# Kernel optimization log

Measured on AMD Instinct MI355X. Metric: run time of the kernel, lower is better.

Reference implementation:

```python
import jax, jax.numpy as jnp
import numpy as np

B, S, HQ, HKV, DH = 1, 2048, 32, 8, 128
DE = HQ * DH  # DEmbed = 4096
G = HQ // HKV  # GQA group size = 4


def apply_rope(x, cs):
    # x: [B, S, H, DH]; cs: [2, S, 1, DH//2] (broadcast over B via leading dims)
    d = x.shape[-1] // 2
    x1, x2 = x[..., :d], x[..., d:]
    y1 = x1 * cs[0] + x2 * cs[1]
    y2 = -x1 * cs[1] + x2 * cs[0]
    return jnp.concatenate([y1, y2], axis=-1)


def setup_inputs() -> dict:
    key = jax.random.key(0)
    ks = jax.random.split(key, 5)
    x = jax.random.normal(ks[0], (B, S, DE), dtype=jnp.float32)
    # Precomputed rotary tables, shaped [2, S, 1, DH//2] so they broadcast over [B,S,H,DH//2]
    half = DH // 2
    inv_freq = 1.0 / (10000.0 ** (np.arange(half, dtype=np.float64) / half))
    ang = np.arange(S, dtype=np.float64)[:, None] * inv_freq[None, :]
    cos_sin_RoPE = jnp.asarray(
        np.stack([np.cos(ang), np.sin(ang)])[:, :, None, :], dtype=jnp.float32
    )
    sc = DE ** -0.5
    wq = jax.random.normal(ks[1], (DE, HQ * DH), dtype=jnp.float32) * sc
    wk = jax.random.normal(ks[2], (DE, HKV * DH), dtype=jnp.float32) * sc
    wv = jax.random.normal(ks[3], (DE, HKV * DH), dtype=jnp.float32) * sc
    wo = jax.random.normal(ks[4], (DE, DE), dtype=jnp.float32) * sc
    return {"x": x, "cos_sin_RoPE": cos_sin_RoPE, "wq": wq, "wk": wk, "wv": wv, "wo": wo}


def reference(x, cos_sin_RoPE, wq, wk, wv, wo):
    b, s, _ = x.shape
    q = (x @ wq).reshape(b, s, HQ, DH)
    k = (x @ wk).reshape(b, s, HKV, DH)
    v = (x @ wv).reshape(b, s, HKV, DH)
    q = apply_rope(q, cos_sin_RoPE)
    k = apply_rope(k, cos_sin_RoPE)
    # GQA causal SDPA: group query heads per kv head
    q = q.transpose(0, 2, 1, 3).reshape(b, HKV, G, s, DH)  # [b,kv,g,s,d]
    k = k.transpose(0, 2, 1, 3)  # [b,kv,s,d]
    v = v.transpose(0, 2, 1, 3)  # [b,kv,s,d]
    scale = DH ** -0.5
    scores = jnp.einsum('bkgsd,bktd->bkgst', q, k) * scale  # [b,kv,g,s,s]
    mask = jnp.tril(jnp.ones((s, s), dtype=bool))
    scores = jnp.where(mask, scores, jnp.finfo(scores.dtype).min)
    p = jax.nn.softmax(scores, axis=-1)
    o = jnp.einsum('bkgst,bktd->bkgsd', p, v)  # [b,kv,g,s,d]
    o = o.transpose(0, 3, 1, 2, 4).reshape(b, s, HQ * DH)
    return o @ wo
```

## Files before the change

### kernel.cpp

```cpp
#include <hip/hip_runtime.h>
#include <hip/hip_bf16.h>
#include <cstdint>
#include <cstddef>

typedef __bf16 bf16x8 __attribute__((ext_vector_type(8)));
typedef float floatx4 __attribute__((ext_vector_type(4)));

#define MFMA(a, b, c) __builtin_amdgcn_mfma_f32_16x16x32_bf16((a), (b), (c), 0, 0, 0)
#define WAITVM(N) asm volatile("s_waitcnt vmcnt(" #N ")" ::: "memory")
#define WAITLGKM0() asm volatile("s_waitcnt lgkmcnt(0)" ::: "memory")
#define BARRIER() do { asm volatile("" ::: "memory"); __builtin_amdgcn_s_barrier(); asm volatile("" ::: "memory"); } while (0)
#define SCHEDBAR() __builtin_amdgcn_sched_barrier(0)

__device__ __forceinline__ unsigned short f2bf(float f) {
  unsigned u = __builtin_bit_cast(unsigned, f);
  u += 0x7fffu + ((u >> 16) & 1u);
  return (unsigned short)(u >> 16);
}
__device__ __forceinline__ float bf2f(unsigned short h) {
  unsigned u = ((unsigned)h) << 16;
  return __builtin_bit_cast(float, u);
}
__device__ __forceinline__ float fast_exp2(float x) {
#if __has_builtin(__builtin_amdgcn_exp2f)
  return __builtin_amdgcn_exp2f(x);
#else
  return exp2f(x);
#endif
}

__device__ __forceinline__ void gl2lds16(const unsigned short* g, unsigned short* l) {
  __builtin_amdgcn_global_load_lds(
      (const __attribute__((address_space(1))) unsigned int*)g,
      (__attribute__((address_space(3))) unsigned int*)l, 16, 0, 0);
}

__global__ void convert_f32_bf16(const float* __restrict__ src,
                                 unsigned short* __restrict__ dst, int n4) {
  int i = blockIdx.x * 256 + threadIdx.x;
  if (i >= n4) return;
  float4 f = ((const float4*)src)[i];
  ushort4 o;
  o.x = f2bf(f.x); o.y = f2bf(f.y); o.z = f2bf(f.z); o.w = f2bf(f.w);
  ((ushort4*)dst)[i] = o;
}

__global__ void transpose_f32_bf16(const float* __restrict__ src,
                                   unsigned short* __restrict__ dst, int K, int N) {
  __shared__ float tile[64 * 65];
  int tn = blockIdx.x * 64, tk = blockIdx.y * 64;
  int r = threadIdx.x >> 4;
  int c4 = (threadIdx.x & 15) * 4;
#pragma unroll
  for (int i = 0; i < 4; i++) {
    float4 f = *(const float4*)&src[(size_t)(tk + r + 16 * i) * N + tn + c4];
    float* tr = &tile[(r + 16 * i) * 65 + c4];
    tr[0] = f.x; tr[1] = f.y; tr[2] = f.z; tr[3] = f.w;
  }
  __syncthreads();
#pragma unroll
  for (int i = 0; i < 4; i++) {
    ushort4 o;
    o.x = f2bf(tile[(c4 + 0) * 65 + r + 16 * i]);
    o.y = f2bf(tile[(c4 + 1) * 65 + r + 16 * i]);
    o.z = f2bf(tile[(c4 + 2) * 65 + r + 16 * i]);
    o.w = f2bf(tile[(c4 + 3) * 65 + r + 16 * i]);
    *(ushort4*)&dst[(size_t)(tn + r + 16 * i) * K + tk + c4] = o;
  }
}

template <int MI, int NI, bool F32OUT>
__global__ __launch_bounds__(512, 2) void gemm_pipe(
    const unsigned short* __restrict__ A,
    const unsigned short* __restrict__ Bt,
    void* __restrict__ C, int M, int N, int K) {
  constexpr int BM = MI * 32;
  constexpr int BN = NI * 64;
  constexpr int NCA = BM / 64;
  __shared__ alignas(16) unsigned short Al[2][BM * 64];
  __shared__ alignas(16) unsigned short Bl[2][BN * 64];
  const int tid = threadIdx.x;
  const int w = tid >> 6, L = tid & 63;
  const int lr = L & 15, lg = L >> 4, lr7 = lr & 7;
  const int bm = blockIdx.y * BM, bn = blockIdx.x * BN;
  const int wm = (w >> 2) * (MI * 16);
  const int wn = (w & 3) * (NI * 16);
  const int NT = K >> 6;

  const int srow = tid >> 3, scg = tid & 7;
  const unsigned short* Ag = &A[(size_t)(bm + srow) * K + ((scg ^ (srow & 7)) * 8)];
  const unsigned short* Bg = &Bt[(size_t)(bn + srow) * K + ((scg ^ (srow & 7)) * 8)];
  unsigned short* AlT = &Al[0][0] + tid * 8;
  unsigned short* BlT = &Bl[0][0] + tid * 8;

#pragma unroll
  for (int t = 0; t < 2; ++t) {
#pragma unroll
    for (int c = 0; c < NCA; ++c)
      gl2lds16(Ag + (size_t)(c * 64) * K + t * 64, AlT + t * (BM * 64) + c * 4096);
#pragma unroll
    for (int c = 0; c < NI; ++c)
      gl2lds16(Bg + (size_t)(c * 64) * K + t * 64, BlT + t * (BN * 64) + c * 4096);
  }

  floatx4 acc[MI][NI] = {};

#define CLUSTER(MLO, KK)                                                    \
  do {                                                                      \
    __builtin_amdgcn_s_setprio(1);                                          \
    _Pragma("unroll") for (int mi = 0; mi < 4; ++mi)                        \
        _Pragma("unroll") for (int ni = 0; ni < NI; ++ni)                   \
            acc[(MLO) + mi][ni] =                                           \
        MFMA(af[(MLO) + mi][KK], bq[ni][KK], acc[(MLO) + mi][ni]);          \
    __builtin_amdgcn_s_setprio(0);                                          \
  } while (0)

  if constexpr (NCA + NI == 7) WAITVM(7); else WAITVM(6);
  BARRIER();

  for (int T = 0; T < NT; ++T) {
    const int buf = T & 1;
    const unsigned short* Ab = &Al[buf][0];
    const unsigned short* Bb = &Bl[buf][0];
    const bool st = (T + 2) < NT;
    const size_t kofs = (size_t)(T + 2) * 64;
    unsigned short* Ad = AlT + buf * (BM * 64);
    unsigned short* Bd = BlT + buf * (BN * 64);

    bf16x8 af[MI][2], bq[NI][2];
#pragma unroll
    for (int mi = 0; mi < MI; ++mi) {
      af[mi][0] = *(const bf16x8*)&Ab[(wm + mi * 16 + lr) * 64 + ((lg ^ lr7) * 8)];
      af[mi][1] = *(const bf16x8*)&Ab[(wm + mi * 16 + lr) * 64 + (((4 + lg) ^ lr7) * 8)];
    }
#pragma unroll
    for (int ni = 0; ni < NI; ++ni) {
      bq[ni][0] = *(const bf16x8*)&Bb[(wn + ni * 16 + lr) * 64 + ((lg ^ lr7) * 8)];
      bq[ni][1] = *(const bf16x8*)&Bb[(wn + ni * 16 + lr) * 64 + (((4 + lg) ^ lr7) * 8)];
    }

    if constexpr (MI == 8) {
      CLUSTER(0, 0);
      WAITLGKM0();
      BARRIER(); SCHEDBAR();
      if (st) {
        gl2lds16(Ag + kofs, Ad);
        gl2lds16(Ag + (size_t)64 * K + kofs, Ad + 4096);
        gl2lds16(Ag + (size_t)128 * K + kofs, Ad + 2 * 4096);
      }
      CLUSTER(4, 0);
      BARRIER(); SCHEDBAR();
      if (st) {
        gl2lds16(Ag + (size_t)192 * K + kofs, Ad + 3 * 4096);
        gl2lds16(Bg + kofs, Bd);
        if constexpr (NI >= 2) gl2lds16(Bg + (size_t)64 * K + kofs, Bd + 4096);
      }
      CLUSTER(0, 1);
      BARRIER(); SCHEDBAR();
      if (st) {
#pragma unroll
        for (int c = 2; c < NI; ++c)
          gl2lds16(Bg + (size_t)(c * 64) * K + kofs, Bd + c * 4096);
      }
      CLUSTER(4, 1);
      if constexpr (NCA + NI == 7) { if (st) { WAITVM(7); } else if (T + 1 < NT) { WAITVM(0); } }
      else                         { if (st) { WAITVM(6); } else if (T + 1 < NT) { WAITVM(0); } }
      BARRIER(); SCHEDBAR();
    } else {
      CLUSTER(0, 0);
      WAITLGKM0();
      BARRIER(); SCHEDBAR();
      if (st) {
#pragma unroll
        for (int c = 0; c < NCA; ++c)
          gl2lds16(Ag + (size_t)(c * 64) * K + kofs, Ad + c * 4096);
#pragma unroll
        for (int c = 0; c < NI; ++c)
          gl2lds16(Bg + (size_t)(c * 64) * K + kofs, Bd + c * 4096);
      }
      CLUSTER(0, 1);
      if constexpr (NCA + NI == 7) { if (st) { WAITVM(7); } else if (T + 1 < NT) { WAITVM(0); } }
      else                         { if (st) { WAITVM(6); } else if (T + 1 < NT) { WAITVM(0); } }
      BARRIER(); SCHEDBAR();
    }
  }
#undef CLUSTER

#pragma unroll
  for (int mi = 0; mi < MI; ++mi) {
#pragma unroll
    for (int ni = 0; ni < NI; ++ni) {
#pragma unroll
      for (int r = 0; r < 4; ++r) {
        size_t row = bm + wm + mi * 16 + lg * 4 + r;
        size_t col = bn + wn + ni * 16 + lr;
        float v = acc[mi][ni][r];
        if constexpr (F32OUT) ((float*)C)[row * N + col] = v;
        else ((unsigned short*)C)[row * N + col] = f2bf(v);
      }
    }
  }
}

__global__ void rope_kernel(unsigned short* __restrict__ X, const float* __restrict__ cs,
                            int H, int rowStride, int colOff, float scale) {
  int idx = blockIdx.x * 256 + threadIdx.x;
  int dg = idx & 15;
  int h = (idx >> 4) % H;
  int s = idx / (16 * H);
  size_t base = (size_t)s * rowStride + colOff + (size_t)h * 128 + dg * 4;
  ushort4 xa = *(const ushort4*)&X[base];
  ushort4 xb = *(const ushort4*)&X[base + 64];
  float4 c = *(const float4*)&cs[s * 64 + dg * 4];
  float4 sn = *(const float4*)&cs[2048 * 64 + s * 64 + dg * 4];
  ushort4 oa, ob;
  {
    float x1 = bf2f(xa.x), x2 = bf2f(xb.x);
    oa.x = f2bf((x1 * c.x + x2 * sn.x) * scale);
    ob.x = f2bf((x2 * c.x - x1 * sn.x) * scale);
  }
  {
    float x1 = bf2f(xa.y), x2 = bf2f(xb.y);
    oa.y = f2bf((x1 * c.y + x2 * sn.y) * scale);
    ob.y = f2bf((x2 * c.y - x1 * sn.y) * scale);
  }
  {
    float x1 = bf2f(xa.z), x2 = bf2f(xb.z);
    oa.z = f2bf((x1 * c.z + x2 * sn.z) * scale);
    ob.z = f2bf((x2 * c.z - x1 * sn.z) * scale);
  }
  {
    float x1 = bf2f(xa.w), x2 = bf2f(xb.w);
    oa.w = f2bf((x1 * c.w + x2 * sn.w) * scale);
    ob.w = f2bf((x2 * c.w - x1 * sn.w) * scale);
  }
  *(ushort4*)&X[base] = oa;
  *(ushort4*)&X[base + 64] = ob;
}

__global__ void v_transpose(const unsigned short* __restrict__ QKV,
                            unsigned short* __restrict__ Vt) {
  __shared__ unsigned short tile[32][33];
  int h = blockIdx.z;
  int s0 = blockIdx.x * 32, d0 = blockIdx.y * 32;
  int c = threadIdx.x & 31, r0 = threadIdx.x >> 5;
#pragma unroll
  for (int i = 0; i < 32; i += 8)
    tile[r0 + i][c] = QKV[(size_t)(s0 + r0 + i) * 6144 + 5120 + h * 128 + d0 + c];
  __syncthreads();
#pragma unroll
  for (int i = 0; i < 32; i += 8)
    Vt[(size_t)(h * 128 + d0 + r0 + i) * 2048 + s0 + c] = tile[c][r0 + i];
}

__global__ __launch_bounds__(256) void flash_kernel(
    const unsigned short* __restrict__ QKV,
    const unsigned short* __restrict__ Vt,
    unsigned short* __restrict__ O) {
  constexpr int PSTR = 72;
  __shared__ alignas(16) unsigned short Klds[64 * 128];
  __shared__ alignas(16) unsigned short Vlds[128 * 64];
  __shared__ alignas(16) unsigned short Plds[4 * 32 * PSTR];
  const int tid = threadIdx.x, w = tid >> 6, L = tid & 63;
  const int lr = L & 15, lg = L >> 4;
  const int bid = blockIdx.x;
  const int hk = bid & 7;
  const int hp = (bid >> 3) & 1;
  const int qb = 31 - (bid >> 4);
  const int hq = hk * 4 + hp * 2 + (w & 1);
  const int qr0 = qb * 64 + (w >> 1) * 32;
  const unsigned short* Kg = QKV + 4096;

  const int k_row = tid >> 4, k_lcg = tid & 15;
  const unsigned short* KgT = &Kg[(size_t)k_row * 6144 + hk * 128 + ((k_lcg ^ (k_row & 15)) * 8)];
  unsigned short* KlT = &Klds[k_row * 128 + k_lcg * 8];
  const int v_row = tid >> 3, v_lcg = tid & 7;
  const unsigned short* VgT = &Vt[(size_t)(hk * 128 + v_row) * 2048 + ((v_lcg ^ (v_row & 7)) * 8)];
  unsigned short* VlT = &Vlds[v_row * 64 + v_lcg * 8];

  bf16x8 qf[2][4];
#pragma unroll
  for (int mi = 0; mi < 2; mi++)
#pragma unroll
    for (int c = 0; c < 4; c++)
      qf[mi][c] = *(const bf16x8*)&QKV[(size_t)(qr0 + mi * 16 + lr) * 6144 + hq * 128 + c * 32 + lg * 8];

  floatx4 oacc[2][8] = {};
  float l_lane[2][4] = {};
  unsigned short* pw = &Plds[w * 32 * PSTR];

  for (int t = 0; t <= qb; t++) {
    const int kv0 = t * 64;
    __syncthreads();
#pragma unroll
    for (int i = 0; i < 4; i++) {
      gl2lds16(KgT + (size_t)(kv0 + i * 16) * 6144, KlT + i * 16 * 128);
      gl2lds16(VgT + kv0 + (size_t)(i * 32) * 2048, VlT + i * 32 * 64);
    }
    __syncthreads();

#pragma unroll
    for (int nt = 0; nt < 4; nt++) {
      bf16x8 kf[4];
#pragma unroll
      for (int c = 0; c < 4; c++)
        kf[c] = *(const bf16x8*)&Klds[(nt * 16 + lr) * 128 + (((c * 4 + lg) ^ lr) * 8)];
      floatx4 sc[2];
#pragma unroll
      for (int mi = 0; mi < 2; mi++) {
        floatx4 a = {};
#pragma unroll
        for (int c = 0; c < 4; c++) a = MFMA(qf[mi][c], kf[c], a);
        sc[mi] = a;
      }
      if (t == qb) {
#pragma unroll
        for (int mi = 0; mi < 2; mi++)
#pragma unroll
          for (int r = 0; r < 4; r++)
            if (kv0 + nt * 16 + lr > qr0 + mi * 16 + lg * 4 + r) sc[mi][r] = -3e38f;
      }
#pragma unroll
      for (int mi = 0; mi < 2; mi++)
#pragma unroll
        for (int r = 0; r < 4; r++) {
          float p = fast_exp2(sc[mi][r]);
          l_lane[mi][r] += p;
          pw[(mi * 16 + lg * 4 + r) * PSTR + nt * 16 + lr] = f2bf(p);
        }
    }

    bf16x8 pf[2][2];
#pragma unroll
    for (int mi = 0; mi < 2; mi++)
#pragma unroll
      for (int c = 0; c < 2; c++)
        pf[mi][c] = *(const bf16x8*)&pw[(mi * 16 + lr) * PSTR + c * 32 + lg * 8];

#pragma unroll
    for (int n = 0; n < 8; n++) {
#pragma unroll
      for (int c = 0; c < 2; c++) {
        bf16x8 vf = *(const bf16x8*)&Vlds[(n * 16 + lr) * 64 + (((c * 4 + lg) ^ (lr & 7)) * 8)];
#pragma unroll
        for (int mi = 0; mi < 2; mi++) oacc[mi][n] = MFMA(pf[mi][c], vf, oacc[mi][n]);
      }
    }
  }

  float linv[2][4];
#pragma unroll
  for (int mi = 0; mi < 2; mi++)
#pragma unroll
    for (int r = 0; r < 4; r++) {
      float l = l_lane[mi][r];
      l += __shfl_xor(l, 1);
      l += __shfl_xor(l, 2);
      l += __shfl_xor(l, 4);
      l += __shfl_xor(l, 8);
      linv[mi][r] = 1.0f / l;
    }

#pragma unroll
  for (int mi = 0; mi < 2; mi++)
#pragma unroll
    for (int n = 0; n < 8; n++)
#pragma unroll
      for (int r = 0; r < 4; r++) {
        size_t row = qr0 + mi * 16 + lg * 4 + r;
        size_t col = (size_t)hq * 128 + n * 16 + lr;
        O[row * 4096 + col] = f2bf(oacc[mi][n][r] * linv[mi][r]);
      }
}

extern "C" void kernel_launch(void* const* d_in, const int* in_sizes, int n_in,
                              void* d_out, int out_size, void* d_ws, size_t ws_size,
                              hipStream_t stream) {
  const float* x  = (const float*)d_in[0];
  const float* cs = (const float*)d_in[1];
  const float* wq = (const float*)d_in[2];
  const float* wk = (const float*)d_in[3];
  const float* wv = (const float*)d_in[4];
  const float* wo = (const float*)d_in[5];
  float* out = (float*)d_out;

  char* ws = (char*)d_ws;
  unsigned short* xb   = (unsigned short*)(ws);
  unsigned short* wqt  = (unsigned short*)(ws + 16777216);
  unsigned short* wkt  = (unsigned short*)(ws + 50331648);
  unsigned short* wvt  = (unsigned short*)(ws + 58720256);
  unsigned short* wot  = (unsigned short*)(ws + 67108864);
  unsigned short* QKVb = (unsigned short*)(ws + 100663296);
  unsigned short* Vtb  = (unsigned short*)(ws + 125829120);
  unsigned short* Ob   = xb;

  convert_f32_bf16<<<8192, 256, 0, stream>>>(x, xb, 2097152);
  transpose_f32_bf16<<<dim3(64, 64), 256, 0, stream>>>(wq, wqt, 4096, 4096);
  transpose_f32_bf16<<<dim3(16, 64), 256, 0, stream>>>(wk, wkt, 4096, 1024);
  transpose_f32_bf16<<<dim3(16, 64), 256, 0, stream>>>(wv, wvt, 4096, 1024);
  transpose_f32_bf16<<<dim3(64, 64), 256, 0, stream>>>(wo, wot, 4096, 4096);

  gemm_pipe<8, 3, false><<<dim3(32, 8), 512, 0, stream>>>(xb, wqt, QKVb, 2048, 6144, 4096);

  rope_kernel<<<4096, 256, 0, stream>>>(QKVb, cs, 32, 6144, 0, 0.12751743f);
  rope_kernel<<<1024, 256, 0, stream>>>(QKVb, cs, 8, 6144, 4096, 1.0f);

  v_transpose<<<dim3(64, 4, 8), 256, 0, stream>>>(QKVb, Vtb);

  flash_kernel<<<512, 256, 0, stream>>>(QKVb, Vtb, Ob);

  gemm_pipe<4, 4, true><<<dim3(16, 16), 512, 0, stream>>>(Ob, wot, out, 2048, 4096, 4096);
}
```

Before: 488.5 us.

## Interleave LDS fragment loads with MFMA clusters and reassign warp column mapping

Restructures the GEMM main loop so LDS fragment reads are issued in stages between MFMA clusters instead of all up front. Each stage is followed by a wait and barrier, and global-to-LDS prefetches are redistributed across the stages. In the non-MI8 variant, each warp now owns strided columns (stride 64) instead of a contiguous block, and it loads B fragments one column at a time. The aim is to cut register pressure and hide LDS latency behind MFMA work, at the cost of more barriers per iteration and removed sched_barriers.

```diff
diff --git a/kernel.cpp b/kernel.cpp
--- a/kernel.cpp
+++ b/kernel.cpp
@@ -10,7 +10,6 @@
 #define WAITVM(N) asm volatile("s_waitcnt vmcnt(" #N ")" ::: "memory")
 #define WAITLGKM0() asm volatile("s_waitcnt lgkmcnt(0)" ::: "memory")
 #define BARRIER() do { asm volatile("" ::: "memory"); __builtin_amdgcn_s_barrier(); asm volatile("" ::: "memory"); } while (0)
-#define SCHEDBAR() __builtin_amdgcn_sched_barrier(0)
 
 __device__ __forceinline__ unsigned short f2bf(float f) {
   unsigned u = __builtin_bit_cast(unsigned, f);
@@ -77,6 +76,7 @@
   constexpr int BM = MI * 32;
   constexpr int BN = NI * 64;
   constexpr int NCA = BM / 64;
+  constexpr int CSTEP = (MI == 8) ? 16 : 64;
   __shared__ alignas(16) unsigned short Al[2][BM * 64];
   __shared__ alignas(16) unsigned short Bl[2][BN * 64];
   const int tid = threadIdx.x;
@@ -84,7 +84,7 @@
   const int lr = L & 15, lg = L >> 4, lr7 = lr & 7;
   const int bm = blockIdx.y * BM, bn = blockIdx.x * BN;
   const int wm = (w >> 2) * (MI * 16);
-  const int wn = (w & 3) * (NI * 16);
+  const int wn = (w & 3) * ((MI == 8) ? (NI * 16) : 16);
   const int NT = K >> 6;
 
   const int srow = tid >> 3, scg = tid & 7;
@@ -105,15 +105,8 @@
 
   floatx4 acc[MI][NI] = {};
 
-#define CLUSTER(MLO, KK)                                                    \
-  do {                                                                      \
-    __builtin_amdgcn_s_setprio(1);                                          \
-    _Pragma("unroll") for (int mi = 0; mi < 4; ++mi)                        \
-        _Pragma("unroll") for (int ni = 0; ni < NI; ++ni)                   \
-            acc[(MLO) + mi][ni] =                                           \
-        MFMA(af[(MLO) + mi][KK], bq[ni][KK], acc[(MLO) + mi][ni]);          \
-    __builtin_amdgcn_s_setprio(0);                                          \
-  } while (0)
+#define LD_A(mi, kk) (*(const bf16x8*)&Ab[(wm + (mi) * 16 + lr) * 64 + ((((kk) * 4 + lg) ^ lr7) * 8)])
+#define LD_B(ni, kk) (*(const bf16x8*)&Bb[(wn + (ni) * CSTEP + lr) * 64 + ((((kk) * 4 + lg) ^ lr7) * 8)])
 
   if constexpr (NCA + NI == 7) WAITVM(7); else WAITVM(6);
   BARRIER();
@@ -126,65 +119,121 @@
     const size_t kofs = (size_t)(T + 2) * 64;
     unsigned short* Ad = AlT + buf * (BM * 64);
     unsigned short* Bd = BlT + buf * (BN * 64);
-
     bf16x8 af[MI][2], bq[NI][2];
-#pragma unroll
-    for (int mi = 0; mi < MI; ++mi) {
-      af[mi][0] = *(const bf16x8*)&Ab[(wm + mi * 16 + lr) * 64 + ((lg ^ lr7) * 8)];
-      af[mi][1] = *(const bf16x8*)&Ab[(wm + mi * 16 + lr) * 64 + (((4 + lg) ^ lr7) * 8)];
-    }
-#pragma unroll
-    for (int ni = 0; ni < NI; ++ni) {
-      bq[ni][0] = *(const bf16x8*)&Bb[(wn + ni * 16 + lr) * 64 + ((lg ^ lr7) * 8)];
-      bq[ni][1] = *(const bf16x8*)&Bb[(wn + ni * 16 + lr) * 64 + (((4 + lg) ^ lr7) * 8)];
-    }
 
     if constexpr (MI == 8) {
-      CLUSTER(0, 0);
-      WAITLGKM0();
-      BARRIER(); SCHEDBAR();
+#pragma unroll
+      for (int mi = 0; mi < 4; ++mi) af[mi][0] = LD_A(mi, 0);
+#pragma unroll
+      for (int ni = 0; ni < NI; ++ni) bq[ni][0] = LD_B(ni, 0);
+      WAITLGKM0(); BARRIER();
+      __builtin_amdgcn_s_setprio(1);
+#pragma unroll
+      for (int mi = 0; mi < 4; ++mi)
+#pragma unroll
+        for (int ni = 0; ni < NI; ++ni)
+          acc[mi][ni] = MFMA(af[mi][0], bq[ni][0], acc[mi][ni]);
+      __builtin_amdgcn_s_setprio(0);
+#pragma unroll
+      for (int mi = 4; mi < 8; ++mi) af[mi][0] = LD_A(mi, 0);
+#pragma unroll
+      for (int ni = 0; ni < NI; ++ni) bq[ni][1] = LD_B(ni, 1);
+      WAITLGKM0(); BARRIER();
+      __builtin_amdgcn_s_setprio(1);
+#pragma unroll
+      for (int mi = 4; mi < 8; ++mi)
+#pragma unroll
+        for (int ni = 0; ni < NI; ++ni)
+          acc[mi][ni] = MFMA(af[mi][0], bq[ni][0], acc[mi][ni]);
+      __builtin_amdgcn_s_setprio(0);
+#pragma unroll
+      for (int mi = 0; mi < 8; ++mi) af[mi][1] = LD_A(mi, 1);
+      if (st) {
+#pragma unroll
+        for (int c = 0; c < NI; ++c)
+          gl2lds16(Bg + (size_t)(c * 64) * K + kofs, Bd + c * 4096);
+      }
+      WAITLGKM0(); BARRIER();
+      __builtin_amdgcn_s_setprio(1);
+#pragma unroll
+      for (int mi = 0; mi < 4; ++mi)
+#pragma unroll
+        for (int ni = 0; ni < NI; ++ni)
+          acc[mi][ni] = MFMA(af[mi][1], bq[ni][1], acc[mi][ni]);
+      __builtin_amdgcn_s_setprio(0);
+      if (st) {
+#pragma unroll
+        for (int c = 0; c < NCA; ++c)
+          gl2lds16(Ag + (size_t)(c * 64) * K + kofs, Ad + c * 4096);
+      }
+      BARRIER();
+      __builtin_amdgcn_s_setprio(1);
+#pragma unroll
+      for (int mi = 4; mi < 8; ++mi)
+#pragma unroll
+        for (int ni = 0; ni < NI; ++ni)
+          acc[mi][ni] = MFMA(af[mi][1], bq[ni][1], acc[mi][ni]);
+      __builtin_amdgcn_s_setprio(0);
+    } else {
+#pragma unroll
+      for (int mi = 0; mi < 4; ++mi) {
+        af[mi][0] = LD_A(mi, 0);
+        af[mi][1] = LD_A(mi, 1);
+      }
+      bq[0][0] = LD_B(0, 0); bq[0][1] = LD_B(0, 1);
+      WAITLGKM0(); BARRIER();
+      __builtin_amdgcn_s_setprio(1);
+#pragma unroll
+      for (int kk = 0; kk < 2; ++kk)
+#pragma unroll
+        for (int mi = 0; mi < 4; ++mi)
+          acc[mi][0] = MFMA(af[mi][kk], bq[0][kk], acc[mi][0]);
+      __builtin_amdgcn_s_setprio(0);
+      bq[1][0] = LD_B(1, 0); bq[1][1] = LD_B(1, 1);
       if (st) {
         gl2lds16(Ag + kofs, Ad);
         gl2lds16(Ag + (size_t)64 * K + kofs, Ad + 4096);
-        gl2lds16(Ag + (size_t)128 * K + kofs, Ad + 2 * 4096);
-      }
-      CLUSTER(4, 0);
-      BARRIER(); SCHEDBAR();
+        gl2lds16(Bg + kofs, Bd);
+      }
+      WAITLGKM0(); BARRIER();
+      __builtin_amdgcn_s_setprio(1);
+#pragma unroll
+      for (int kk = 0; kk < 2; ++kk)
+#pragma unroll
+        for (int mi = 0; mi < 4; ++mi)
+          acc[mi][1] = MFMA(af[mi][kk], bq[1][kk], acc[mi][1]);
+      __builtin_amdgcn_s_setprio(0);
+      bq[2][0] = LD_B(2, 0); bq[2][1] = LD_B(2, 1);
+      bq[3][0] = LD_B(3, 0); bq[3][1] = LD_B(3, 1);
+      if (st) gl2lds16(Bg + (size_t)64 * K + kofs, Bd + 4096);
+      WAITLGKM0(); BARRIER();
+      __builtin_amdgcn_s_setprio(1);
+#pragma unroll
+      for (int kk = 0; kk < 2; ++kk)
+#pragma unroll
+        for (int mi = 0; mi < 4; ++mi)
+          acc[mi][2] = MFMA(af[mi][kk], bq[2][kk], acc[mi][2]);
+      __builtin_amdgcn_s_setprio(0);
       if (st) {
-        gl2lds16(Ag + (size_t)192 * K + kofs, Ad + 3 * 4096);
-        gl2lds16(Bg + kofs, Bd);
-        if constexpr (NI >= 2) gl2lds16(Bg + (size_t)64 * K + kofs, Bd + 4096);
-      }
-      CLUSTER(0, 1);
-      BARRIER(); SCHEDBAR();
-      if (st) {
-#pragma unroll
-        for (int c = 2; c < NI; ++c)
-          gl2lds16(Bg + (size_t)(c * 64) * K + kofs, Bd + c * 4096);
-      }
-      CLUSTER(4, 1);
-      if constexpr (NCA + NI == 7) { if (st) { WAITVM(7); } else if (T + 1 < NT) { WAITVM(0); } }
-      else                         { if (st) { WAITVM(6); } else if (T + 1 < NT) { WAITVM(0); } }
-      BARRIER(); SCHEDBAR();
-    } else {
-      CLUSTER(0, 0);
-      WAITLGKM0();
-      BARRIER(); SCHEDBAR();
-      if (st) {
-#pragma unroll
-        for (int c = 0; c < NCA; ++c)
-          gl2lds16(Ag + (size_t)(c * 64) * K + kofs, Ad + c * 4096);
-#pragma unroll
-        for (int c = 0; c < NI; ++c)
-          gl2lds16(Bg + (size_t)(c * 64) * K + kofs, Bd + c * 4096);
-      }
-      CLUSTER(0, 1);
-      if constexpr (NCA + NI == 7) { if (st) { WAITVM(7); } else if (T + 1 < NT) { WAITVM(0); } }
-      else                         { if (st) { WAITVM(6); } else if (T + 1 < NT) { WAITVM(0); } }
-      BARRIER(); SCHEDBAR();
-    }
-  }
-#undef CLUSTER
+        gl2lds16(Bg + (size_t)128 * K + kofs, Bd + 2 * 4096);
+        gl2lds16(Bg + (size_t)192 * K + kofs, Bd + 3 * 4096);
+      }
+      BARRIER();
+      __builtin_amdgcn_s_setprio(1);
+#pragma unroll
+      for (int kk = 0; kk < 2; ++kk)
+#pragma unroll
+        for (int mi = 0; mi < 4; ++mi)
+          acc[mi][3] = MFMA(af[mi][kk], bq[3][kk], acc[mi][3]);
+      __builtin_amdgcn_s_setprio(0);
+    }
+
+    if constexpr (NCA + NI == 7) { if (st) { WAITVM(7); } else if (T + 1 < NT) { WAITVM(0); } }
+    else                         { if (st) { WAITVM(6); } else if (T + 1 < NT) { WAITVM(0); } }
+    BARRIER();
+  }
+#undef LD_A
+#undef LD_B
 
 #pragma unroll
   for (int mi = 0; mi < MI; ++mi) {
@@ -193,7 +242,7 @@
 #pragma unroll
       for (int r = 0; r < 4; ++r) {
         size_t row = bm + wm + mi * 16 + lg * 4 + r;
-        size_t col = bn + wn + ni * 16 + lr;
+        size_t col = bn + wn + ni * CSTEP + lr;
         float v = acc[mi][ni][r];
         if constexpr (F32OUT) ((float*)C)[row * N + col] = v;
         else ((unsigned short*)C)[row * N + col] = f2bf(v);
```

Result: no change. 491.4 us (+0.6%).
